# Optimization experiments

Hardware: AMD Instinct MI355X
Metric: run time of the kernel (lower is better)

## Reference

```python
import jax, jax.numpy as jnp
import numpy as np

HIDDEN = 1024
NUM_HEADS = 16
HEAD_DIM = HIDDEN // NUM_HEADS
ROPE_THETA = 10000.0


def rope_tables(seq_len, head_dim, theta):
    inv_freq = 1.0 / theta ** (jnp.arange(0, head_dim, 2, dtype=jnp.float32) / head_dim)
    pos = jnp.arange(seq_len, dtype=jnp.float32)
    freqs = jnp.outer(pos, inv_freq)  # [S, hd/2]
    return jnp.cos(freqs), jnp.sin(freqs)


def apply_rope(x, cos, sin):
    # x: [B, nh, S, hd]; cos/sin: [S, hd/2]
    x1, x2 = jnp.split(x, 2, axis=-1)
    return jnp.concatenate([x1 * cos - x2 * sin, x2 * cos + x1 * sin], axis=-1)


def setup_inputs() -> dict:
    key = jax.random.key(0)
    k1, k2, k3 = jax.random.split(key, 3)
    B, S = 2, 2048
    hidden_states = jax.random.normal(k1, (B, S, HIDDEN), dtype=jnp.float32)
    # nn.Linear stores weight as [out, in]; y = x @ W.T
    Wqkv = jax.random.normal(k2, (3 * HIDDEN, HIDDEN), dtype=jnp.float32) * (HIDDEN ** -0.5)
    Wo = jax.random.normal(k3, (HIDDEN, HIDDEN), dtype=jnp.float32) * (HIDDEN ** -0.5)
    return {"hidden_states": hidden_states, "Wqkv": Wqkv, "Wo": Wo}


def reference(hidden_states, Wqkv, Wo):
    B, S, H = hidden_states.shape
    qkv = hidden_states @ Wqkv.T  # [B, S, 3H]
    qkv = qkv.reshape(B, S, 3, NUM_HEADS, HEAD_DIM)
    q, k, v = jnp.moveaxis(qkv, 2, 0)  # each [B, S, nh, hd]
    q = jnp.transpose(q, (0, 2, 1, 3))  # [B, nh, S, hd]
    k = jnp.transpose(k, (0, 2, 1, 3))
    v = jnp.transpose(v, (0, 2, 1, 3))
    cos, sin = rope_tables(S, HEAD_DIM, ROPE_THETA)
    q = apply_rope(q, cos, sin)
    k = apply_rope(k, cos, sin)
    scale = 1.0 / jnp.sqrt(jnp.asarray(HEAD_DIM, dtype=q.dtype))
    scores = jnp.einsum("bhqd,bhkd->bhqk", q, k) * scale
    causal = jnp.tril(jnp.ones((S, S), dtype=bool))
    scores = jnp.where(causal, scores, jnp.finfo(scores.dtype).min)
    attn = jax.nn.softmax(scores, axis=-1)
    out = jnp.einsum("bhqk,bhkd->bhqd", attn, v)  # [B, nh, S, hd]
    out = jnp.transpose(out, (0, 2, 1, 3)).reshape(B, S, H)
    return out @ Wo.T
```

## Files before the change

### kernel.cpp

```cpp
#include <hip/hip_runtime.h>
#include <hip/hip_bf16.h>
#include <math.h>

typedef __bf16 bf16_t;
typedef __attribute__((ext_vector_type(8))) __bf16 bf16x8;
typedef __attribute__((ext_vector_type(4))) float f32x4;
typedef __attribute__((ext_vector_type(16))) float f32x16;
typedef __attribute__((ext_vector_type(4))) unsigned u32x4;

#define AS1(p) ((__attribute__((address_space(1))) void*)(p))
#define AS3(p) ((__attribute__((address_space(3))) void*)(p))

__device__ inline unsigned pkbf(float a, float b) {
  bf16_t x = (bf16_t)a, y = (bf16_t)b;
  return (unsigned)__builtin_bit_cast(unsigned short, x) |
         ((unsigned)__builtin_bit_cast(unsigned short, y) << 16);
}
__device__ inline f32x16 zero16() {
  f32x16 z;
#pragma unroll
  for (int r = 0; r < 16; ++r) z[r] = 0.f;
  return z;
}

__device__ inline void cvt8(const float* __restrict__ in, bf16_t* __restrict__ out, int i) {
  const float4* p = (const float4*)in;
  float4 a = p[2 * i], b = p[2 * i + 1];
  bf16x8 o;
  o[0] = (bf16_t)a.x; o[1] = (bf16_t)a.y; o[2] = (bf16_t)a.z; o[3] = (bf16_t)a.w;
  o[4] = (bf16_t)b.x; o[5] = (bf16_t)b.y; o[6] = (bf16_t)b.z; o[7] = (bf16_t)b.w;
  ((bf16x8*)out)[i] = o;
}

__global__ __launch_bounds__(256)
void prep_all(const float* __restrict__ hid, const float* __restrict__ wqkv,
              const float* __restrict__ wo, bf16_t* __restrict__ hidb,
              bf16_t* __restrict__ wqkvb, bf16_t* __restrict__ wob,
              float* __restrict__ cosb, float* __restrict__ sinb) {
  const int bid = blockIdx.x, tid = threadIdx.x;
  if (bid < 2048) {
    cvt8(hid, hidb, bid * 256 + tid);
  } else if (bid < 3584) {
    cvt8(wqkv, wqkvb, (bid - 2048) * 256 + tid);
  } else if (bid < 4096) {
    cvt8(wo, wob, (bid - 3584) * 256 + tid);
  } else {
    int t = (bid - 4096) * 256 + tid;
    int s = t >> 5, i = t & 31;
    float inv = powf(10000.0f, -(float)i / 32.0f);
    float sv, cv;
    sincosf((float)s * inv, &sv, &cv);
    cosb[t] = cv;
    sinb[t] = sv;
  }
}

__global__ __launch_bounds__(256, 2)
void gemm_qkv(const bf16_t* __restrict__ A, const bf16_t* __restrict__ B,
              bf16_t* __restrict__ qkv, bf16_t* __restrict__ Kp,
              const float* __restrict__ cosb, const float* __restrict__ sinb) {
  __shared__ __align__(16) bf16_t lA[128 * 64];
  __shared__ __align__(16) bf16_t lB[128 * 64];
  const int K = 1024;
  const int tid = threadIdx.x;
  const int wid = tid >> 6, lane = tid & 63;
  const int lr = lane & 15, lg = lane >> 4;
  const int nwg = gridDim.x * gridDim.y;
  int lin = blockIdx.y * gridDim.x + blockIdx.x;
  lin = (lin & 7) * (nwg >> 3) + (lin >> 3);
  const int m0 = (lin / gridDim.x) * 128, n0 = (lin % gridDim.x) * 128;
  const int wm = (wid >> 1) * 64, wn = (wid & 1) * 64;
  const int srow = lane >> 3;
  const int scol = (lane & 7) * 8;
  f32x4 acc[4][4];
#pragma unroll
  for (int i = 0; i < 4; ++i)
#pragma unroll
    for (int j = 0; j < 4; ++j) acc[i][j] = f32x4{0.f, 0.f, 0.f, 0.f};

  for (int kt = 0; kt < 16; ++kt) {
    const int k0 = kt << 6;
    __syncthreads();
#pragma unroll
    for (int i = 0; i < 4; ++i) {
      int c = (wid << 2) + i;
      int r = (c << 3) + srow;
      __builtin_amdgcn_global_load_lds(AS1(A + (size_t)(m0 + r) * K + k0 + scol),
                                       AS3(&lA[c * 512]), 16, 0, 0);
      __builtin_amdgcn_global_load_lds(AS1(B + (size_t)(n0 + r) * K + k0 + scol),
                                       AS3(&lB[c * 512]), 16, 0, 0);
    }
    __syncthreads();
#pragma unroll
    for (int ks = 0; ks < 2; ++ks) {
      bf16x8 af[4], bfr[4];
#pragma unroll
      for (int i = 0; i < 4; ++i) {
        af[i]  = *(const bf16x8*)&lA[(wm + i * 16 + lr) * 64 + ks * 32 + lg * 8];
        bfr[i] = *(const bf16x8*)&lB[(wn + i * 16 + lr) * 64 + ks * 32 + lg * 8];
      }
#pragma unroll
      for (int i = 0; i < 4; ++i)
#pragma unroll
        for (int j = 0; j < 4; ++j)
          acc[i][j] = __builtin_amdgcn_mfma_f32_16x16x32_bf16(af[i], bfr[j], acc[i][j], 0, 0, 0);
    }
  }
  const int sec = n0 >> 10;
  const int hcol = ((n0 + wn) & 1023) >> 6;
  if (sec == 2) {
#pragma unroll
    for (int i = 0; i < 4; ++i) {
      int token0 = m0 + wm + i * 16 + lg * 4;
      int bb = token0 >> 11;
      int t = (token0 & 2047) >> 6;
      int kv0 = token0 & 63;
      bf16_t* vd = qkv + ((size_t)(bb * 2048 + t * 64)) * 3072 + 2048 + hcol * 64;
#pragma unroll
      for (int j = 0; j < 4; ++j) {
        int d = j * 16 + lr;
        uint2 w;
        w.x = pkbf(acc[i][j][0], acc[i][j][1]);
        w.y = pkbf(acc[i][j][2], acc[i][j][3]);
        *(uint2*)(vd + (size_t)d * 3072 + (((kv0 >> 3) ^ (d & 7)) * 8) + (kv0 & 7)) = w;
      }
    }
  } else {
    const float SC = sec ? 1.0f : 0.125f * 1.4426950408889634f;
#pragma unroll
    for (int i = 0; i < 4; ++i)
#pragma unroll
      for (int r = 0; r < 4; ++r) {
        int token = m0 + wm + i * 16 + lg * 4 + r;
        int s = token & 2047;
#pragma unroll
        for (int j = 0; j < 2; ++j) {
          int f = j * 16 + lr;
          float cv = cosb[s * 32 + f], sv = sinb[s * 32 + f];
          float x1 = acc[i][j][r], x2 = acc[i][j + 2][r];
          float y1 = (x1 * cv - x2 * sv) * SC;
          float y2 = (x2 * cv + x1 * sv) * SC;
          if (sec == 0) {
            bf16_t* qd = qkv + (size_t)token * 3072 + hcol * 64;
            qd[f] = (bf16_t)y1;
            qd[f + 32] = (bf16_t)y2;
          } else {
            int bb = token >> 11, t = (token & 2047) >> 6, rk = token & 63;
            bf16_t* kd = Kp + ((size_t)((bb * 16 + hcol) * 32 + t)) * 4096 + rk * 64;
            int c1 = f >> 3;
            kd[((c1 ^ (rk & 7)) * 8) + (lr & 7)] = (bf16_t)y1;
            kd[(((c1 + 4) ^ (rk & 7)) * 8) + (lr & 7)] = (bf16_t)y2;
          }
        }
      }
  }
}

__global__ __launch_bounds__(256, 2)
void gemm_nt_f32(const bf16_t* __restrict__ A, const bf16_t* __restrict__ B,
                 float* __restrict__ C, int M, int N, int K) {
  __shared__ __align__(16) bf16_t lA[128 * 64];
  __shared__ __align__(16) bf16_t lB[128 * 64];
  const int tid = threadIdx.x;
  const int wid = tid >> 6, lane = tid & 63;
  const int lr = lane & 15, lg = lane >> 4;
  const int nwg = gridDim.x * gridDim.y;
  int lin = blockIdx.y * gridDim.x + blockIdx.x;
  lin = (lin & 7) * (nwg >> 3) + (lin >> 3);
  const int m0 = (lin / gridDim.x) * 128, n0 = (lin % gridDim.x) * 128;
  const int wm = (wid >> 1) * 64, wn = (wid & 1) * 64;
  const int srow = lane >> 3;
  const int scol = (lane & 7) * 8;
  f32x4 acc[4][4];
#pragma unroll
  for (int i = 0; i < 4; ++i)
#pragma unroll
    for (int j = 0; j < 4; ++j) acc[i][j] = f32x4{0.f, 0.f, 0.f, 0.f};

  const int nk = K >> 6;
  for (int kt = 0; kt < nk; ++kt) {
    const int k0 = kt << 6;
    __syncthreads();
#pragma unroll
    for (int i = 0; i < 4; ++i) {
      int c = (wid << 2) + i;
      int r = (c << 3) + srow;
      __builtin_amdgcn_global_load_lds(AS1(A + (size_t)(m0 + r) * K + k0 + scol),
                                       AS3(&lA[c * 512]), 16, 0, 0);
      __builtin_amdgcn_global_load_lds(AS1(B + (size_t)(n0 + r) * K + k0 + scol),
                                       AS3(&lB[c * 512]), 16, 0, 0);
    }
    __syncthreads();
#pragma unroll
    for (int ks = 0; ks < 2; ++ks) {
      bf16x8 af[4], bfr[4];
#pragma unroll
      for (int i = 0; i < 4; ++i) {
        af[i]  = *(const bf16x8*)&lA[(wm + i * 16 + lr) * 64 + ks * 32 + lg * 8];
        bfr[i] = *(const bf16x8*)&lB[(wn + i * 16 + lr) * 64 + ks * 32 + lg * 8];
      }
#pragma unroll
      for (int i = 0; i < 4; ++i)
#pragma unroll
        for (int j = 0; j < 4; ++j)
          acc[i][j] = __builtin_amdgcn_mfma_f32_16x16x32_bf16(af[i], bfr[j], acc[i][j], 0, 0, 0);
    }
  }
#pragma unroll
  for (int i = 0; i < 4; ++i)
#pragma unroll
    for (int j = 0; j < 4; ++j)
#pragma unroll
      for (int r = 0; r < 4; ++r) {
        int row = m0 + wm + i * 16 + lg * 4 + r;
        int col = n0 + wn + j * 16 + lr;
        C[(size_t)row * N + col] = acc[i][j][r];
      }
}

__device__ const unsigned char ROLE_LUT[44] = {
    19, 18, 17, 16,
    15, 95, 159, 158,
    14, 94, 93, 157,
    13, 92, 156, 91, 155, 154,
    12, 90, 89, 153, 152,
    11, 88, 87, 151, 150,
    10, 86, 85, 149, 148,
    9, 84,
    8, 7, 6, 5, 4, 3, 2, 1, 0};

__global__ __launch_bounds__(128, 2)
void attn_fwd(const bf16_t* __restrict__ qkv, const bf16_t* __restrict__ Kp,
              bf16_t* __restrict__ O, bf16_t* __restrict__ Po, float* __restrict__ Plp) {
  __shared__ __align__(16) bf16_t Ksh[2][4096];
  __shared__ __align__(16) bf16_t Vsh[2][4096];
  const int tid = threadIdx.x, wid = tid >> 6, lane = tid & 63;
  const int ln = lane & 31, h = lane >> 5;
  const int lin = blockIdx.x;
  const int e = ROLE_LUT[lin >> 5];
  const int bh = lin & 31;
  const int c = e & 31, kind = e >> 6;
  const int b = bh >> 4, hd = bh & 15;
  const int t0 = (kind == 2) ? ((c + 1) >> 1) : 0;
  const int t1 = (kind == 1) ? ((c + 1) >> 1) : c + 1;
  const int qw = c * 64 + wid * 32;

  const bf16_t* Qrow = qkv + ((size_t)(b * 2048 + qw + ln)) * 3072 + hd * 64;
  bf16x8 qf[4];
#pragma unroll
  for (int t = 0; t < 4; ++t) qf[t] = *(const bf16x8*)(Qrow + t * 16 + h * 8);

  f32x16 o0 = zero16(), o1 = zero16();
  float lp = 0.f;

  const bf16_t* Kbase = Kp + ((size_t)bh * 32) * 4096 + tid * 8;
  const bf16_t* Vbase = qkv + ((size_t)(b * 2048 + (tid >> 3))) * 3072 + 2048 + hd * 64 + (tid & 7) * 8;

#define STAGE(T, BUF)                                                                     \
  do {                                                                                    \
    const bf16_t* ks = Kbase + (size_t)(T) * 4096;                                        \
    __builtin_amdgcn_global_load_lds(AS1(ks),        AS3(&Ksh[BUF][tid * 8]), 16, 0, 0);  \
    __builtin_amdgcn_global_load_lds(AS1(ks + 1024), AS3(&Ksh[BUF][1024 + tid * 8]), 16, 0, 0); \
    __builtin_amdgcn_global_load_lds(AS1(ks + 2048), AS3(&Ksh[BUF][2048 + tid * 8]), 16, 0, 0); \
    __builtin_amdgcn_global_load_lds(AS1(ks + 3072), AS3(&Ksh[BUF][3072 + tid * 8]), 16, 0, 0); \
    const bf16_t* vs = Vbase + (size_t)(T) * 64 * 3072;                                   \
    __builtin_amdgcn_global_load_lds(AS1(vs),             AS3(&Vsh[BUF][tid * 8]), 16, 0, 0);        \
    __builtin_amdgcn_global_load_lds(AS1(vs + 16 * 3072), AS3(&Vsh[BUF][1024 + tid * 8]), 16, 0, 0); \
    __builtin_amdgcn_global_load_lds(AS1(vs + 32 * 3072), AS3(&Vsh[BUF][2048 + tid * 8]), 16, 0, 0); \
    __builtin_amdgcn_global_load_lds(AS1(vs + 48 * 3072), AS3(&Vsh[BUF][3072 + tid * 8]), 16, 0, 0); \
  } while (0)

  STAGE(t0, t0 & 1);
  for (int t = t0; t < t1; ++t) {
    asm volatile("s_waitcnt vmcnt(0)" ::: "memory");
    __builtin_amdgcn_s_barrier();
    if (t + 1 < t1) STAGE(t + 1, (t + 1) & 1);
    const bf16_t* K = &Ksh[t & 1][0];
    const bf16_t* V = &Vsh[t & 1][0];
    f32x16 s0 = zero16(), s1 = zero16();
    __builtin_amdgcn_s_setprio(1);
#pragma unroll
    for (int u = 0; u < 4; ++u) {
      const int ch = 2 * u + h;
      bf16x8 k0 = *(const bf16x8*)&K[ln * 64 + ((ch ^ (ln & 7)) * 8)];
      bf16x8 k1 = *(const bf16x8*)&K[(32 + ln) * 64 + ((ch ^ (ln & 7)) * 8)];
      s0 = __builtin_amdgcn_mfma_f32_32x32x16_bf16(k0, qf[u], s0, 0, 0, 0);
      s1 = __builtin_amdgcn_mfma_f32_32x32x16_bf16(k1, qf[u], s1, 0, 0, 0);
    }
    __builtin_amdgcn_s_setprio(0);
    if (t == c) {
      const int qg = qw + ln, k0g = t * 64;
#pragma unroll
      for (int r = 0; r < 16; ++r) {
        int kv = k0g + (r & 3) + 8 * (r >> 2) + 4 * h;
        if (kv > qg) s0[r] = -3e38f;
        if (kv + 32 > qg) s1[r] = -3e38f;
      }
    }
#pragma unroll
    for (int r = 0; r < 16; ++r) {
      float p0 = __builtin_amdgcn_exp2f(s0[r]); lp += p0; s0[r] = p0;
      float p1 = __builtin_amdgcn_exp2f(s1[r]); lp += p1; s1[r] = p1;
    }
    __builtin_amdgcn_s_setprio(1);
#pragma unroll
    for (int u = 0; u < 4; ++u) {
      const int w = u & 1;
      f32x16 sv = (u >> 1) ? s1 : s0;
      unsigned x  = pkbf(sv[8 * w + 0], sv[8 * w + 1]);
      unsigned x2 = pkbf(sv[8 * w + 2], sv[8 * w + 3]);
      unsigned y  = pkbf(sv[8 * w + 4], sv[8 * w + 5]);
      unsigned y2 = pkbf(sv[8 * w + 6], sv[8 * w + 7]);
      asm volatile("v_permlane32_swap_b32 %0, %1" : "+v"(x), "+v"(y));
      asm volatile("v_permlane32_swap_b32 %0, %1" : "+v"(x2), "+v"(y2));
      u32x4 pw; pw[0] = x; pw[1] = x2; pw[2] = y; pw[3] = y2;
      bf16x8 pf = __builtin_bit_cast(bf16x8, pw);
      const int ch = 2 * u + h;
      bf16x8 v0 = *(const bf16x8*)&V[ln * 64 + ((ch ^ (ln & 7)) * 8)];
      bf16x8 v1 = *(const bf16x8*)&V[(32 + ln) * 64 + ((ch ^ (ln & 7)) * 8)];
      o0 = __builtin_amdgcn_mfma_f32_32x32x16_bf16(v0, pf, o0, 0, 0, 0);
      o1 = __builtin_amdgcn_mfma_f32_32x32x16_bf16(v1, pf, o1, 0, 0, 0);
    }
    __builtin_amdgcn_s_setprio(0);
  }
#undef STAGE
  float lpf = lp + __shfl_xor(lp, 32, 64);
  if (kind == 0) {
    float inv = 1.0f / lpf;
    bf16_t* Oaddr = O + ((size_t)(b * 2048 + qw + ln)) * 1024 + hd * 64;
#pragma unroll
    for (int D = 0; D < 2; ++D) {
      f32x16 ov = D ? o1 : o0;
#pragma unroll
      for (int Q = 0; Q < 4; ++Q) {
        uint2 w;
        w.x = pkbf(ov[4 * Q + 0] * inv, ov[4 * Q + 1] * inv);
        w.y = pkbf(ov[4 * Q + 2] * inv, ov[4 * Q + 3] * inv);
        *(uint2*)(Oaddr + D * 32 + Q * 8 + 4 * h) = w;
      }
    }
  } else {
    const int slot = (bh * 12 + (c - 20)) * 2 + (kind - 1);
    const int qi = wid * 32 + ln;
    if (h == 0) Plp[slot * 64 + qi] = lpf;
    bf16_t* Paddr = Po + ((size_t)(slot * 64 + qi)) * 64;
#pragma unroll
    for (int D = 0; D < 2; ++D) {
      f32x16 ov = D ? o1 : o0;
#pragma unroll
      for (int Q = 0; Q < 4; ++Q) {
        uint2 w;
        w.x = pkbf(ov[4 * Q + 0], ov[4 * Q + 1]);
        w.y = pkbf(ov[4 * Q + 2], ov[4 * Q + 3]);
        *(uint2*)(Paddr + D * 32 + Q * 8 + 4 * h) = w;
      }
    }
  }
}

__global__ __launch_bounds__(64)
void attn_combine(const bf16_t* __restrict__ Po, const float* __restrict__ Plp,
                  bf16_t* __restrict__ O) {
  const int blk = blockIdx.x;
  const int bh = blk / 12, sc = blk % 12;
  const int b = bh >> 4, hd = bh & 15;
  const int c = 20 + sc;
  const int q = threadIdx.x;
  const int slotA = (bh * 12 + sc) * 2, slotB = slotA + 1;
  float inv = 1.0f / (Plp[slotA * 64 + q] + Plp[slotB * 64 + q]);
  const bf16x8* pa = (const bf16x8*)(Po + ((size_t)(slotA * 64 + q)) * 64);
  const bf16x8* pb = (const bf16x8*)(Po + ((size_t)(slotB * 64 + q)) * 64);
  bf16_t* oaddr = O + ((size_t)(b * 2048 + c * 64 + q)) * 1024 + hd * 64;
#pragma unroll
  for (int j = 0; j < 8; ++j) {
    bf16x8 a = pa[j], v = pb[j];
    bf16x8 w;
#pragma unroll
    for (int k = 0; k < 8; ++k) w[k] = (bf16_t)(((float)a[k] + (float)v[k]) * inv);
    ((bf16x8*)oaddr)[j] = w;
  }
}

extern "C" void kernel_launch(void* const* d_in, const int* in_sizes, int n_in,
                              void* d_out, int out_size, void* d_ws, size_t ws_size,
                              hipStream_t stream) {
  const float* hid  = (const float*)d_in[0];
  const float* wqkv = (const float*)d_in[1];
  const float* wo   = (const float*)d_in[2];
  float* out = (float*)d_out;
  char* ws = (char*)d_ws;
  bf16_t* hidb  = (bf16_t*)(ws);
  bf16_t* wqkvb = (bf16_t*)(ws + 8388608);
  bf16_t* wob   = (bf16_t*)(ws + 14680064);
  bf16_t* qkvb  = (bf16_t*)(ws + 16777216);
  float*  cosb  = (float*)(ws + 41943040);
  float*  sinb  = (float*)(ws + 42205184);
  bf16_t* Ob    = (bf16_t*)(ws + 42467328);
  bf16_t* Kp    = (bf16_t*)(ws + 52428800);
  bf16_t* Po    = (bf16_t*)(ws + 60817408);
  float*  Plp   = (float*)(ws + 67108864);

  prep_all<<<4352, 256, 0, stream>>>(hid, wqkv, wo, hidb, wqkvb, wob, cosb, sinb);
  gemm_qkv<<<dim3(24, 32), 256, 0, stream>>>(hidb, wqkvb, qkvb, Kp, cosb, sinb);
  attn_fwd<<<1408, 128, 0, stream>>>(qkvb, Kp, Ob, Po, Plp);
  attn_combine<<<384, 64, 0, stream>>>(Po, Plp, Ob);
  gemm_nt_f32<<<dim3(8, 32), 256, 0, stream>>>(Ob, wob, out, 4096, 1024, 1024);
}
```

Baseline: 115.1 us.

## Double-buffer LDS tiles in QKV and output projection GEMMs

Both projection GEMMs now use two LDS buffers per operand and prefetch the next K tile with global_load_lds while MFMAs run on the current tile. Explicit vmcnt waits and raw s_barrier replace the two __syncthreads per iteration. The goal is to hide global load latency behind compute. In exchange LDS use doubles to 64KB per block, which may limit occupancy at launch_bounds(256,2), and the manual waitcnt and barrier ordering has to be exactly right.

```diff
diff --git a/kernel.cpp b/kernel.cpp
--- a/kernel.cpp
+++ b/kernel.cpp
@@ -59,8 +59,8 @@
 void gemm_qkv(const bf16_t* __restrict__ A, const bf16_t* __restrict__ B,
               bf16_t* __restrict__ qkv, bf16_t* __restrict__ Kp,
               const float* __restrict__ cosb, const float* __restrict__ sinb) {
-  __shared__ __align__(16) bf16_t lA[128 * 64];
-  __shared__ __align__(16) bf16_t lB[128 * 64];
+  __shared__ __align__(16) bf16_t lA[2][128 * 64];
+  __shared__ __align__(16) bf16_t lB[2][128 * 64];
   const int K = 1024;
   const int tid = threadIdx.x;
   const int wid = tid >> 6, lane = tid & 63;
@@ -78,26 +78,37 @@
 #pragma unroll
     for (int j = 0; j < 4; ++j) acc[i][j] = f32x4{0.f, 0.f, 0.f, 0.f};
 
+#define GSTAGE(KT, BUF)                                                                    \
+  do {                                                                                     \
+    const int k0_ = (KT) << 6;                                                             \
+    _Pragma("unroll")                                                                      \
+    for (int i_ = 0; i_ < 4; ++i_) {                                                       \
+      int c_ = (wid << 2) + i_;                                                            \
+      int r_ = (c_ << 3) + srow;                                                           \
+      __builtin_amdgcn_global_load_lds(AS1(A + (size_t)(m0 + r_) * K + k0_ + scol),        \
+                                       AS3(&lA[BUF][c_ * 512]), 16, 0, 0);                 \
+      __builtin_amdgcn_global_load_lds(AS1(B + (size_t)(n0 + r_) * K + k0_ + scol),        \
+                                       AS3(&lB[BUF][c_ * 512]), 16, 0, 0);                 \
+    }                                                                                      \
+  } while (0)
+
+  GSTAGE(0, 0);
   for (int kt = 0; kt < 16; ++kt) {
-    const int k0 = kt << 6;
-    __syncthreads();
-#pragma unroll
-    for (int i = 0; i < 4; ++i) {
-      int c = (wid << 2) + i;
-      int r = (c << 3) + srow;
-      __builtin_amdgcn_global_load_lds(AS1(A + (size_t)(m0 + r) * K + k0 + scol),
-                                       AS3(&lA[c * 512]), 16, 0, 0);
-      __builtin_amdgcn_global_load_lds(AS1(B + (size_t)(n0 + r) * K + k0 + scol),
-                                       AS3(&lB[c * 512]), 16, 0, 0);
-    }
-    __syncthreads();
+    const int buf = kt & 1;
+    if (kt < 15) {
+      GSTAGE(kt + 1, buf ^ 1);
+      asm volatile("s_waitcnt vmcnt(8)" ::: "memory");
+    } else {
+      asm volatile("s_waitcnt vmcnt(0)" ::: "memory");
+    }
+    __builtin_amdgcn_s_barrier();
 #pragma unroll
     for (int ks = 0; ks < 2; ++ks) {
       bf16x8 af[4], bfr[4];
 #pragma unroll
       for (int i = 0; i < 4; ++i) {
-        af[i]  = *(const bf16x8*)&lA[(wm + i * 16 + lr) * 64 + ks * 32 + lg * 8];
-        bfr[i] = *(const bf16x8*)&lB[(wn + i * 16 + lr) * 64 + ks * 32 + lg * 8];
+        af[i]  = *(const bf16x8*)&lA[buf][(wm + i * 16 + lr) * 64 + ks * 32 + lg * 8];
+        bfr[i] = *(const bf16x8*)&lB[buf][(wn + i * 16 + lr) * 64 + ks * 32 + lg * 8];
       }
 #pragma unroll
       for (int i = 0; i < 4; ++i)
@@ -105,7 +116,9 @@
         for (int j = 0; j < 4; ++j)
           acc[i][j] = __builtin_amdgcn_mfma_f32_16x16x32_bf16(af[i], bfr[j], acc[i][j], 0, 0, 0);
     }
-  }
+    __builtin_amdgcn_s_barrier();
+  }
+#undef GSTAGE
   const int sec = n0 >> 10;
   const int hcol = ((n0 + wn) & 1023) >> 6;
   if (sec == 2) {
@@ -159,8 +172,8 @@
 __global__ __launch_bounds__(256, 2)
 void gemm_nt_f32(const bf16_t* __restrict__ A, const bf16_t* __restrict__ B,
                  float* __restrict__ C, int M, int N, int K) {
-  __shared__ __align__(16) bf16_t lA[128 * 64];
-  __shared__ __align__(16) bf16_t lB[128 * 64];
+  __shared__ __align__(16) bf16_t lA[2][128 * 64];
+  __shared__ __align__(16) bf16_t lB[2][128 * 64];
   const int tid = threadIdx.x;
   const int wid = tid >> 6, lane = tid & 63;
   const int lr = lane & 15, lg = lane >> 4;
@@ -177,27 +190,38 @@
 #pragma unroll
     for (int j = 0; j < 4; ++j) acc[i][j] = f32x4{0.f, 0.f, 0.f, 0.f};
 
+#define GSTAGE(KT, BUF)                                                                    \
+  do {                                                                                     \
+    const int k0_ = (KT) << 6;                                                             \
+    _Pragma("unroll")                                                                      \
+    for (int i_ = 0; i_ < 4; ++i_) {                                                       \
+      int c_ = (wid << 2) + i_;                                                            \
+      int r_ = (c_ << 3) + srow;                                                           \
+      __builtin_amdgcn_global_load_lds(AS1(A + (size_t)(m0 + r_) * K + k0_ + scol),        \
+                                       AS3(&lA[BUF][c_ * 512]), 16, 0, 0);                 \
+      __builtin_amdgcn_global_load_lds(AS1(B + (size_t)(n0 + r_) * K + k0_ + scol),        \
+                                       AS3(&lB[BUF][c_ * 512]), 16, 0, 0);                 \
+    }                                                                                      \
+  } while (0)
+
   const int nk = K >> 6;
+  GSTAGE(0, 0);
   for (int kt = 0; kt < nk; ++kt) {
-    const int k0 = kt << 6;
-    __syncthreads();
-#pragma unroll
-    for (int i = 0; i < 4; ++i) {
-      int c = (wid << 2) + i;
-      int r = (c << 3) + srow;
-      __builtin_amdgcn_global_load_lds(AS1(A + (size_t)(m0 + r) * K + k0 + scol),
-                                       AS3(&lA[c * 512]), 16, 0, 0);
-      __builtin_amdgcn_global_load_lds(AS1(B + (size_t)(n0 + r) * K + k0 + scol),
-                                       AS3(&lB[c * 512]), 16, 0, 0);
-    }
-    __syncthreads();
+    const int buf = kt & 1;
+    if (kt + 1 < nk) {
+      GSTAGE(kt + 1, buf ^ 1);
+      asm volatile("s_waitcnt vmcnt(8)" ::: "memory");
+    } else {
+      asm volatile("s_waitcnt vmcnt(0)" ::: "memory");
+    }
+    __builtin_amdgcn_s_barrier();
 #pragma unroll
     for (int ks = 0; ks < 2; ++ks) {
       bf16x8 af[4], bfr[4];
 #pragma unroll
       for (int i = 0; i < 4; ++i) {
-        af[i]  = *(const bf16x8*)&lA[(wm + i * 16 + lr) * 64 + ks * 32 + lg * 8];
-        bfr[i] = *(const bf16x8*)&lB[(wn + i * 16 + lr) * 64 + ks * 32 + lg * 8];
+        af[i]  = *(const bf16x8*)&lA[buf][(wm + i * 16 + lr) * 64 + ks * 32 + lg * 8];
+        bfr[i] = *(const bf16x8*)&lB[buf][(wn + i * 16 + lr) * 64 + ks * 32 + lg * 8];
       }
 #pragma unroll
       for (int i = 0; i < 4; ++i)
@@ -205,7 +229,9 @@
         for (int j = 0; j < 4; ++j)
           acc[i][j] = __builtin_amdgcn_mfma_f32_16x16x32_bf16(af[i], bfr[j], acc[i][j], 0, 0, 0);
     }
-  }
+    __builtin_amdgcn_s_barrier();
+  }
+#undef GSTAGE
 #pragma unroll
   for (int i = 0; i < 4; ++i)
 #pragma unroll
```

Result: slower. 130.2 us (+13.1%).
